# Kernel optimization log

Measured on AMD Instinct MI355X. Metric: run time of the kernel, lower is better.

## Reference

```python
import jax, jax.numpy as jnp
import numpy as np

EPS_SIM = 1e-10
EPS_NORM = 1e-12


def setup_inputs() -> dict:
    key = jax.random.key(0)
    k1, k2, k3, k4, k5 = jax.random.split(key, 5)
    B, CH, H, W = 64, 512, 28, 28
    R = CH // 16  # reduction
    x = jax.random.normal(k1, (B, CH, H, W), dtype=jnp.float32)
    # torch nn.Linear weights are [out, in]
    wD = jax.random.normal(k2, (R, CH), dtype=jnp.float32) * (1.0 / np.sqrt(CH))
    bD = jax.random.normal(k3, (R,), dtype=jnp.float32) * 0.01
    wU = jax.random.normal(k4, (CH, R), dtype=jnp.float32) * (1.0 / np.sqrt(R))
    bU = jax.random.normal(k5, (CH,), dtype=jnp.float32) * 0.01
    return {"x": x, "wD": wD, "bD": bD, "wU": wU, "bU": bU}


def _hybrid_weight(xap):
    # xap: [B, CH, N]; returns row-diag-masked, globally normalized similarity Wij [B, CH, CH]
    gram = jnp.einsum('bin,bjn->bij', xap, xap)           # [B,CH,CH]
    sq = jnp.sum(xap * xap, axis=-1)                      # [B,CH]
    d2 = sq[:, :, None] + sq[:, None, :] - 2.0 * gram
    d = jnp.sqrt(d2)
    d = jnp.where(jnp.isnan(d), 0.0, d)                   # NaN mask (sqrt of negatives)
    d = jnp.maximum(d, 0.0)                               # clamp(0, inf)
    mean_d = jnp.mean(d, axis=(1, 2), keepdims=True)
    l2_sim = jnp.exp(-d / (mean_d + EPS_SIM))
    w = jnp.sqrt(sq)                                      # per-channel L2 norm
    denom = jnp.maximum(w[:, :, None] * w[:, None, :], EPS_SIM)
    cos = gram / denom
    cos = jnp.where(jnp.isnan(cos), 0.0, cos)
    cos = jnp.maximum(cos, 0.0)
    sim = cos * l2_sim
    CH = sim.shape[1]
    sim = sim * (1.0 - jnp.eye(CH, dtype=sim.dtype))      # zero diagonal
    Wij = sim / (jnp.sum(sim, axis=(1, 2), keepdims=True) + EPS_SIM)
    return Wij


def reference(x, wD, bD, wU, bU):
    B, CH, H, W = x.shape
    r = 7  # rdim[512]
    # adaptive avg pool to 7x7 (H, W divisible by 7 -> exact block average)
    xap = x.reshape(B, CH, r, H // r, r, W // r).mean(axis=(3, 5)).reshape(B, CH, r * r)
    Wij = jax.lax.stop_gradient(_hybrid_weight(xap))      # computed under no_grad in torch
    gap = x.mean(axis=(2, 3))                             # [B,CH] global avg pool
    mu = gap.mean(axis=1, keepdims=True)
    std = jnp.std(gap, axis=1, ddof=1, keepdims=True)     # torch std is unbiased
    z = (gap - mu) / std                                  # [B,CH]
    # diag(z z^T Wij)_i = z_i * (z^T Wij)_i  -> avoid materializing zz^T
    local_mi = z * jnp.einsum('bj,bji->bi', z, Wij)       # [B,CH]
    m = local_mi.mean(axis=1, keepdims=True)
    s = jnp.std(local_mi, axis=1, ddof=1, keepdims=True)
    ch = (local_mi - m) / (s + EPS_NORM)                  # normal_G
    h = jax.nn.relu(ch @ wD.T + bD)
    att = h @ wU.T + bU
    scale = jax.nn.sigmoid(att)[:, :, None, None]
    return x * scale
```

## Files before the change

kernel.cpp:

```cpp
#include <hip/hip_runtime.h>
#include <hip/hip_bf16.h>
#include <stdint.h>

#define NB 64
#define NC 512
#define NHW 784
#define NK 49
#define KP 64
#define NR 32
#define NTASK 10

typedef short sh8 __attribute__((ext_vector_type(8)));
typedef float f32x4 __attribute__((ext_vector_type(4)));
typedef int v4i __attribute__((ext_vector_type(4)));

__device__ __forceinline__ float wave_sum(float v) {
#pragma unroll
  for (int o = 32; o; o >>= 1) v += __shfl_xor(v, o);
  return v;
}

__device__ __forceinline__ void task_decode(int s, int& ti, int& tj) {
  if (s < 4) { ti = 0; tj = s; }
  else if (s < 7) { ti = 1; tj = s - 3; }
  else if (s < 9) { ti = 2; tj = s - 5; }
  else { ti = 3; tj = 3; }
}

__global__ __launch_bounds__(256) void pool_kernel(const float* __restrict__ x,
                                                   __hip_bfloat16* __restrict__ xap,
                                                   float* __restrict__ wbuf,
                                                   float* __restrict__ gap) {
  __shared__ float sf[4][196];
  int t = threadIdx.x, wid = t >> 6, lane = t & 63;
  int row = blockIdx.x * 4 + wid;
  const f32x4* xr = (const f32x4*)(x + (size_t)row * NHW);
  f32x4 v0 = xr[lane];
  f32x4 v1 = xr[lane + 64];
  f32x4 v2 = xr[lane + 128];
  sf[wid][lane] = (v0.x + v0.y) + (v0.z + v0.w);
  sf[wid][lane + 64] = (v1.x + v1.y) + (v1.z + v1.w);
  sf[wid][lane + 128] = (v2.x + v2.y) + (v2.z + v2.w);
  if (lane < 4) {
    f32x4 v3 = xr[lane + 192];
    sf[wid][lane + 192] = (v3.x + v3.y) + (v3.z + v3.w);
  }
  __syncthreads();
  float bin = 0.f;
  if (lane < NK) {
    int pr = lane / 7, pc = lane - pr * 7;
    int f0 = pr * 28 + pc;
    bin = ((sf[wid][f0] + sf[wid][f0 + 7]) + (sf[wid][f0 + 14] + sf[wid][f0 + 21])) * 0.0625f;
  }
  float s1 = wave_sum(bin);
  float s2 = wave_sum(bin * bin);
  xap[(size_t)row * KP + lane] = __float2bfloat16(bin);
  if (lane == 0) {
    wbuf[row] = sqrtf(s2);
    gap[row] = s1 * (1.f / 49.f);
  }
}

__global__ __launch_bounds__(256) void meand_kernel(const __hip_bfloat16* __restrict__ xap,
                                                    const float* __restrict__ wbuf,
                                                    const float* __restrict__ gap,
                                                    float* __restrict__ dpart,
                                                    float* __restrict__ zbuf) {
  __shared__ __align__(16) __hip_bfloat16 Ab[128 * KP];
  __shared__ __align__(16) __hip_bfloat16 Bb[128 * KP];
  __shared__ float wiL[128], wjL[128];
  __shared__ float red[4];
  int blk = blockIdx.x;
  int b = blk / NTASK, s = blk - b * NTASK;
  int ti, tj;
  task_decode(s, ti, tj);
  bool diag = (ti == tj);
  int i0 = ti * 128, j0 = tj * 128;
  int t = threadIdx.x;
  int lane = t & 63, wave = t >> 6;
  const v4i* ga = (const v4i*)(xap + ((size_t)b * NC + i0) * KP);
  const v4i* gb = (const v4i*)(xap + ((size_t)b * NC + j0) * KP);
  v4i* la = (v4i*)Ab;
  v4i* lb = (v4i*)Bb;
#pragma unroll
  for (int q = 0; q < 4; ++q) {
    int cid = q * 256 + t;
    int r = cid >> 3, c = cid & 7;
    int dst = (r << 3) | (c ^ (r & 7));
    la[dst] = ga[cid];
    lb[dst] = gb[cid];
  }
  if (t < 128) {
    wiL[t] = wbuf[b * NC + i0 + t];
    wjL[t] = wbuf[b * NC + j0 + t];
  }
  if (s == 0) {
    float g0 = gap[b * NC + t], g1 = gap[b * NC + t + 256];
    float s1 = wave_sum(g0 + g1);
    if (lane == 0) red[wave] = s1;
    __syncthreads();
    float mu = ((red[0] + red[1]) + (red[2] + red[3])) * (1.f / 512.f);
    float e0 = g0 - mu, e1 = g1 - mu;
    __syncthreads();
    float vv = wave_sum(e0 * e0 + e1 * e1);
    if (lane == 0) red[wave] = vv;
    __syncthreads();
    float inv_sd = __builtin_amdgcn_rsqf(((red[0] + red[1]) + (red[2] + red[3])) * (1.f / 511.f));
    zbuf[b * NC + t] = e0 * inv_sd;
    zbuf[b * NC + t + 256] = e1 * inv_sd;
  }
  __syncthreads();
  int wi = wave >> 1, wn = wave & 1;
  int l15 = lane & 15, g16 = lane >> 4;
  sh8 af[4][2], bfr[4][2];
#pragma unroll
  for (int f = 0; f < 4; ++f) {
#pragma unroll
    for (int ks = 0; ks < 2; ++ks) {
      int ra = wi * 64 + f * 16 + l15;
      int rb = wn * 64 + f * 16 + l15;
      int cg2 = ks * 4 + g16;
      af[f][ks] = __builtin_bit_cast(sh8, ((const v4i*)Ab)[(ra << 3) | (cg2 ^ (ra & 7))]);
      bfr[f][ks] = __builtin_bit_cast(sh8, ((const v4i*)Bb)[(rb << 3) | (cg2 ^ (rb & 7))]);
    }
  }
  f32x4 acc[4][4];
#pragma unroll
  for (int fm = 0; fm < 4; ++fm)
#pragma unroll
    for (int fn = 0; fn < 4; ++fn) acc[fm][fn] = (f32x4){0.f, 0.f, 0.f, 0.f};
#pragma unroll
  for (int ks = 0; ks < 2; ++ks)
#pragma unroll
    for (int fm = 0; fm < 4; ++fm)
#pragma unroll
      for (int fn = 0; fn < 4; ++fn)
        acc[fm][fn] =
            __builtin_amdgcn_mfma_f32_16x16x32_bf16(af[fm][ks], bfr[fn][ks], acc[fm][fn], 0, 0, 0);
  float a2[4][4], b2[4];
#pragma unroll
  for (int fm = 0; fm < 4; ++fm)
#pragma unroll
    for (int rg = 0; rg < 4; ++rg) {
      float a = wiL[wi * 64 + fm * 16 + g16 * 4 + rg];
      a2[fm][rg] = a * a;
    }
#pragma unroll
  for (int fn = 0; fn < 4; ++fn) {
    float w = wjL[wn * 64 + fn * 16 + l15];
    b2[fn] = w * w;
  }
  float dsum = 0.f;
#pragma unroll
  for (int fm = 0; fm < 4; ++fm)
#pragma unroll
    for (int fn = 0; fn < 4; ++fn)
#pragma unroll
      for (int rg = 0; rg < 4; ++rg) {
        float d2 = fmaf(-2.f, acc[fm][fn][rg], a2[fm][rg] + b2[fn]);
        dsum += __builtin_amdgcn_sqrtf(fmaxf(d2, 0.f));
      }
  dsum = wave_sum(dsum);
  __syncthreads();
  if (lane == 0) red[wave] = dsum;
  __syncthreads();
  if (t == 0) dpart[blk] = ((red[0] + red[1]) + (red[2] + red[3])) * (diag ? 1.f : 2.f);
}

__global__ __launch_bounds__(256) void sim_kernel(const __hip_bfloat16* __restrict__ xap,
                                                  const float* __restrict__ wbuf,
                                                  const float* __restrict__ zbuf,
                                                  const float* __restrict__ dpart,
                                                  float* __restrict__ tpart,
                                                  float* __restrict__ spart) {
  __shared__ __align__(16) __hip_bfloat16 Ab[128 * KP];
  __shared__ __align__(16) __hip_bfloat16 Bb[128 * KP];
  __shared__ float wiL[128], wjL[128], zL[NC], tfull[NC];
  __shared__ float red[4];
  int blk = blockIdx.x;
  int b = blk / NTASK, s = blk - b * NTASK;
  int ti, tj;
  task_decode(s, ti, tj);
  bool diag = (ti == tj);
  int i0 = ti * 128, j0 = tj * 128;
  int t = threadIdx.x;
  int lane = t & 63, wave = t >> 6;
  float dsb = 0.f;
#pragma unroll
  for (int k = 0; k < NTASK; ++k) dsb += dpart[b * NTASK + k];
  float nim = -1.44269504f / (dsb * (1.f / 262144.f) + 1e-10f);
  const v4i* ga = (const v4i*)(xap + ((size_t)b * NC + i0) * KP);
  const v4i* gb = (const v4i*)(xap + ((size_t)b * NC + j0) * KP);
  v4i* la = (v4i*)Ab;
  v4i* lb = (v4i*)Bb;
#pragma unroll
  for (int q = 0; q < 4; ++q) {
    int cid = q * 256 + t;
    int r = cid >> 3, c = cid & 7;
    int dst = (r << 3) | (c ^ (r & 7));
    la[dst] = ga[cid];
    lb[dst] = gb[cid];
  }
  if (t < 128) {
    wiL[t] = wbuf[b * NC + i0 + t];
    wjL[t] = wbuf[b * NC + j0 + t];
  }
  zL[t] = zbuf[b * NC + t];
  zL[t + 256] = zbuf[b * NC + t + 256];
  tfull[t] = 0.f;
  tfull[t + 256] = 0.f;
  __syncthreads();
  int wi = wave >> 1, wn = wave & 1;
  int l15 = lane & 15, g16 = lane >> 4;
  sh8 af[4][2], bfr[4][2];
#pragma unroll
  for (int f = 0; f < 4; ++f) {
#pragma unroll
    for (int ks = 0; ks < 2; ++ks) {
      int ra = wi * 64 + f * 16 + l15;
      int rb = wn * 64 + f * 16 + l15;
      int cg2 = ks * 4 + g16;
      af[f][ks] = __builtin_bit_cast(sh8, ((const v4i*)Ab)[(ra << 3) | (cg2 ^ (ra & 7))]);
      bfr[f][ks] = __builtin_bit_cast(sh8, ((const v4i*)Bb)[(rb << 3) | (cg2 ^ (rb & 7))]);
    }
  }
  f32x4 acc[4][4];
#pragma unroll
  for (int fm = 0; fm < 4; ++fm)
#pragma unroll
    for (int fn = 0; fn < 4; ++fn) acc[fm][fn] = (f32x4){0.f, 0.f, 0.f, 0.f};
#pragma unroll
  for (int ks = 0; ks < 2; ++ks)
#pragma unroll
    for (int fm = 0; fm < 4; ++fm)
#pragma unroll
      for (int fn = 0; fn < 4; ++fn)
        acc[fm][fn] =
            __builtin_amdgcn_mfma_f32_16x16x32_bf16(af[fm][ks], bfr[fn][ks], acc[fm][fn], 0, 0, 0);
  float a2[4][4], ia[4][4], zi[4][4];
#pragma unroll
  for (int fm = 0; fm < 4; ++fm)
#pragma unroll
    for (int rg = 0; rg < 4; ++rg) {
      int il = wi * 64 + fm * 16 + g16 * 4 + rg;
      float a = wiL[il];
      a2[fm][rg] = a * a;
      ia[fm][rg] = __builtin_amdgcn_rcpf(fmaxf(a, 1e-7f));
      zi[fm][rg] = zL[i0 + il];
    }
  float b2[4], ib[4], zj[4];
#pragma unroll
  for (int fn = 0; fn < 4; ++fn) {
    int jl = wn * 64 + fn * 16 + l15;
    float w = wjL[jl];
    b2[fn] = w * w;
    ib[fn] = __builtin_amdgcn_rcpf(fmaxf(w, 1e-7f));
    zj[fn] = zL[j0 + jl];
  }
  float ssum = 0.f;
  float trow[4][4];
  float tcol[4] = {0.f, 0.f, 0.f, 0.f};
#pragma unroll
  for (int fm = 0; fm < 4; ++fm)
#pragma unroll
    for (int rg = 0; rg < 4; ++rg) trow[fm][rg] = 0.f;
#pragma unroll
  for (int fm = 0; fm < 4; ++fm)
#pragma unroll
    for (int fn = 0; fn < 4; ++fn) {
      float ibn = ib[fn];
#pragma unroll
      for (int rg = 0; rg < 4; ++rg) {
        float g = acc[fm][fn][rg];
        float d2 = fmaf(-2.f, g, a2[fm][rg] + b2[fn]);
        float d = __builtin_amdgcn_sqrtf(fmaxf(d2, 0.f));
        float sim = fmaxf(g, 0.f) * ia[fm][rg] * ibn * exp2f(d * nim);
        if (diag) {
          int il = wi * 64 + fm * 16 + g16 * 4 + rg;
          int jl = wn * 64 + fn * 16 + l15;
          if (il == jl) sim = 0.f;
        }
        ssum += sim;
        trow[fm][rg] = fmaf(sim, zj[fn], trow[fm][rg]);
        tcol[fn] = fmaf(sim, zi[fm][rg], tcol[fn]);
      }
    }
#pragma unroll
  for (int fm = 0; fm < 4; ++fm)
#pragma unroll
    for (int rg = 0; rg < 4; ++rg) {
      float v = trow[fm][rg];
#pragma unroll
      for (int o = 8; o; o >>= 1) v += __shfl_xor(v, o);
      if (l15 == 0) atomicAdd(&tfull[i0 + wi * 64 + fm * 16 + g16 * 4 + rg], v);
    }
  if (!diag) {
#pragma unroll
    for (int fn = 0; fn < 4; ++fn) {
      float v = tcol[fn];
      v += __shfl_xor(v, 16);
      v += __shfl_xor(v, 32);
      if (g16 == 0) atomicAdd(&tfull[j0 + wn * 64 + fn * 16 + l15], v);
    }
  }
  ssum = wave_sum(ssum);
  if (lane == 0) red[wave] = ssum;
  __syncthreads();
  if (t == 0) spart[blk] = ((red[0] + red[1]) + (red[2] + red[3])) * (diag ? 1.f : 2.f);
  tpart[(size_t)blk * NC + t] = tfull[t];
  tpart[(size_t)blk * NC + t + 256] = tfull[t + 256];
}

__global__ __launch_bounds__(256) void mlp_kernel(const float* __restrict__ zbuf,
                                                  const float* __restrict__ tpart,
                                                  const float* __restrict__ spart,
                                                  const float* __restrict__ wD,
                                                  const float* __restrict__ bD,
                                                  const float* __restrict__ wU,
                                                  const float* __restrict__ bU,
                                                  float* __restrict__ scl) {
  __shared__ float red[4];
  __shared__ float chL[NC];
  __shared__ float hL[NR];
  int b = blockIdx.x, t = threadIdx.x;
  int lane = t & 63, wid = t >> 6;
  float S = 0.f;
#pragma unroll
  for (int k = 0; k < NTASK; ++k) S += spart[b * NTASK + k];
  float invS = 1.f / (S + 1e-10f);
  float t0 = 0.f, t1 = 0.f;
#pragma unroll
  for (int j = 0; j < NTASK; ++j) {
    t0 += tpart[((size_t)b * NTASK + j) * NC + t];
    t1 += tpart[((size_t)b * NTASK + j) * NC + t + 256];
  }
  float lm0 = zbuf[b * NC + t] * t0 * invS;
  float lm1 = zbuf[b * NC + t + 256] * t1 * invS;
  float s2 = wave_sum(lm0 + lm1);
  if (lane == 0) red[wid] = s2;
  __syncthreads();
  float m = ((red[0] + red[1]) + (red[2] + red[3])) * (1.f / 512.f);
  float d0 = lm0 - m, d1 = lm1 - m;
  __syncthreads();
  float v2 = wave_sum(d0 * d0 + d1 * d1);
  if (lane == 0) red[wid] = v2;
  __syncthreads();
  float isd2 = __builtin_amdgcn_rcpf(
      sqrtf(((red[0] + red[1]) + (red[2] + red[3])) * (1.f / 511.f)) + 1e-12f);
  chL[t] = d0 * isd2;
  chL[t + 256] = d1 * isd2;
  __syncthreads();
  int k = t >> 3, p = t & 7;
  const float* wrow = wD + k * NC + p * 64;
  const float* cp = chL + p * 64;
  float hp = 0.f;
#pragma unroll
  for (int i = 0; i < 64; ++i) hp += wrow[i] * cp[i];
#pragma unroll
  for (int o = 4; o; o >>= 1) hp += __shfl_xor(hp, o);
  if (p == 0) hL[k] = fmaxf(hp + bD[k], 0.f);
  __syncthreads();
#pragma unroll
  for (int u = 0; u < 2; ++u) {
    int c = t + u * 256;
    const float* wrU = wU + c * NR;
    float att = bU[c];
#pragma unroll
    for (int kk = 0; kk < NR; ++kk) att += hL[kk] * wrU[kk];
    scl[b * NC + c] = __builtin_amdgcn_rcpf(1.f + __expf(-att));
  }
}

__global__ __launch_bounds__(256) void scale_kernel(const float* __restrict__ x,
                                                    const float* __restrict__ scl,
                                                    float* __restrict__ out) {
  unsigned idx = blockIdx.x * 256u + threadIdx.x;
  unsigned row = idx / 196u;
  float s = scl[row];
  f32x4 v = ((const f32x4*)x)[idx];
  v *= s;
  __builtin_nontemporal_store(v, ((f32x4*)out) + idx);
}

extern "C" void kernel_launch(void* const* d_in, const int* in_sizes, int n_in,
                              void* d_out, int out_size, void* d_ws, size_t ws_size,
                              hipStream_t stream) {
  const float* x = (const float*)d_in[0];
  const float* wD = (const float*)d_in[1];
  const float* bD = (const float*)d_in[2];
  const float* wU = (const float*)d_in[3];
  const float* bU = (const float*)d_in[4];
  float* out = (float*)d_out;
  char* ws = (char*)d_ws;

  __hip_bfloat16* xap = (__hip_bfloat16*)ws;
  float* fbase = (float*)(ws + (size_t)NB * NC * KP * 2);
  float* wbuf = fbase;
  float* gap = wbuf + NB * NC;
  float* dpart = gap + NB * NC;
  float* spart = dpart + NB * NTASK;
  float* tpart = spart + NB * NTASK;
  float* scl = tpart + NB * NTASK * NC;
  float* zbuf = scl + NB * NC;

  hipLaunchKernelGGL(pool_kernel, dim3(NB * NC / 4), dim3(256), 0, stream, x, xap, wbuf, gap);
  hipLaunchKernelGGL(meand_kernel, dim3(NB * NTASK), dim3(256), 0, stream, xap, wbuf, gap, dpart,
                     zbuf);
  hipLaunchKernelGGL(sim_kernel, dim3(NB * NTASK), dim3(256), 0, stream, xap, wbuf, zbuf, dpart,
                     tpart, spart);
  hipLaunchKernelGGL(mlp_kernel, dim3(NB), dim3(256), 0, stream, zbuf, tpart, spart, wD, bD, wU,
                     bU, scl);
  hipLaunchKernelGGL(scale_kernel, dim3(25088), dim3(256), 0, stream, x, scl, out);
}
```

Before: 82.31 us.

## Fuse distance, similarity and MLP stages into one per-batch kernel

Replaces the meand, sim and mlp kernels with a single 1024-thread block per batch that keeps the pooled bf16 features, z-scores and accumulators in shared memory. The block loops over all ten upper-triangle tiles twice, first for the mean distance and then for the similarity, with block-level reductions in between. This removes two kernel launches and the global partial-sum round-trips. In exchange, only 64 blocks run the middle stage, which lowers parallelism and serialises the tile work inside each block.

```diff
diff --git a/kernel.cpp b/kernel.cpp
--- a/kernel.cpp
+++ b/kernel.cpp
@@ -61,313 +61,263 @@
   }
 }
 
-__global__ __launch_bounds__(256) void meand_kernel(const __hip_bfloat16* __restrict__ xap,
-                                                    const float* __restrict__ wbuf,
-                                                    const float* __restrict__ gap,
-                                                    float* __restrict__ dpart,
-                                                    float* __restrict__ zbuf) {
-  __shared__ __align__(16) __hip_bfloat16 Ab[128 * KP];
-  __shared__ __align__(16) __hip_bfloat16 Bb[128 * KP];
-  __shared__ float wiL[128], wjL[128];
-  __shared__ float red[4];
-  int blk = blockIdx.x;
-  int b = blk / NTASK, s = blk - b * NTASK;
-  int ti, tj;
-  task_decode(s, ti, tj);
-  bool diag = (ti == tj);
-  int i0 = ti * 128, j0 = tj * 128;
-  int t = threadIdx.x;
-  int lane = t & 63, wave = t >> 6;
-  const v4i* ga = (const v4i*)(xap + ((size_t)b * NC + i0) * KP);
-  const v4i* gb = (const v4i*)(xap + ((size_t)b * NC + j0) * KP);
-  v4i* la = (v4i*)Ab;
-  v4i* lb = (v4i*)Bb;
-#pragma unroll
-  for (int q = 0; q < 4; ++q) {
-    int cid = q * 256 + t;
-    int r = cid >> 3, c = cid & 7;
-    int dst = (r << 3) | (c ^ (r & 7));
-    la[dst] = ga[cid];
-    lb[dst] = gb[cid];
-  }
-  if (t < 128) {
-    wiL[t] = wbuf[b * NC + i0 + t];
-    wjL[t] = wbuf[b * NC + j0 + t];
-  }
-  if (s == 0) {
-    float g0 = gap[b * NC + t], g1 = gap[b * NC + t + 256];
-    float s1 = wave_sum(g0 + g1);
-    if (lane == 0) red[wave] = s1;
-    __syncthreads();
-    float mu = ((red[0] + red[1]) + (red[2] + red[3])) * (1.f / 512.f);
-    float e0 = g0 - mu, e1 = g1 - mu;
-    __syncthreads();
-    float vv = wave_sum(e0 * e0 + e1 * e1);
-    if (lane == 0) red[wave] = vv;
-    __syncthreads();
-    float inv_sd = __builtin_amdgcn_rsqf(((red[0] + red[1]) + (red[2] + red[3])) * (1.f / 511.f));
-    zbuf[b * NC + t] = e0 * inv_sd;
-    zbuf[b * NC + t + 256] = e1 * inv_sd;
-  }
-  __syncthreads();
-  int wi = wave >> 1, wn = wave & 1;
-  int l15 = lane & 15, g16 = lane >> 4;
-  sh8 af[4][2], bfr[4][2];
-#pragma unroll
-  for (int f = 0; f < 4; ++f) {
-#pragma unroll
-    for (int ks = 0; ks < 2; ++ks) {
-      int ra = wi * 64 + f * 16 + l15;
-      int rb = wn * 64 + f * 16 + l15;
-      int cg2 = ks * 4 + g16;
-      af[f][ks] = __builtin_bit_cast(sh8, ((const v4i*)Ab)[(ra << 3) | (cg2 ^ (ra & 7))]);
-      bfr[f][ks] = __builtin_bit_cast(sh8, ((const v4i*)Bb)[(rb << 3) | (cg2 ^ (rb & 7))]);
-    }
-  }
-  f32x4 acc[4][4];
-#pragma unroll
-  for (int fm = 0; fm < 4; ++fm)
-#pragma unroll
-    for (int fn = 0; fn < 4; ++fn) acc[fm][fn] = (f32x4){0.f, 0.f, 0.f, 0.f};
-#pragma unroll
-  for (int ks = 0; ks < 2; ++ks)
-#pragma unroll
-    for (int fm = 0; fm < 4; ++fm)
-#pragma unroll
-      for (int fn = 0; fn < 4; ++fn)
-        acc[fm][fn] =
-            __builtin_amdgcn_mfma_f32_16x16x32_bf16(af[fm][ks], bfr[fn][ks], acc[fm][fn], 0, 0, 0);
-  float a2[4][4], b2[4];
-#pragma unroll
-  for (int fm = 0; fm < 4; ++fm)
-#pragma unroll
-    for (int rg = 0; rg < 4; ++rg) {
-      float a = wiL[wi * 64 + fm * 16 + g16 * 4 + rg];
-      a2[fm][rg] = a * a;
-    }
-#pragma unroll
-  for (int fn = 0; fn < 4; ++fn) {
-    float w = wjL[wn * 64 + fn * 16 + l15];
-    b2[fn] = w * w;
-  }
-  float dsum = 0.f;
-#pragma unroll
-  for (int fm = 0; fm < 4; ++fm)
-#pragma unroll
-    for (int fn = 0; fn < 4; ++fn)
-#pragma unroll
-      for (int rg = 0; rg < 4; ++rg) {
-        float d2 = fmaf(-2.f, acc[fm][fn][rg], a2[fm][rg] + b2[fn]);
-        dsum += __builtin_amdgcn_sqrtf(fmaxf(d2, 0.f));
-      }
-  dsum = wave_sum(dsum);
-  __syncthreads();
-  if (lane == 0) red[wave] = dsum;
-  __syncthreads();
-  if (t == 0) dpart[blk] = ((red[0] + red[1]) + (red[2] + red[3])) * (diag ? 1.f : 2.f);
-}
-
-__global__ __launch_bounds__(256) void sim_kernel(const __hip_bfloat16* __restrict__ xap,
-                                                  const float* __restrict__ wbuf,
-                                                  const float* __restrict__ zbuf,
-                                                  const float* __restrict__ dpart,
-                                                  float* __restrict__ tpart,
-                                                  float* __restrict__ spart) {
-  __shared__ __align__(16) __hip_bfloat16 Ab[128 * KP];
-  __shared__ __align__(16) __hip_bfloat16 Bb[128 * KP];
-  __shared__ float wiL[128], wjL[128], zL[NC], tfull[NC];
-  __shared__ float red[4];
-  int blk = blockIdx.x;
-  int b = blk / NTASK, s = blk - b * NTASK;
-  int ti, tj;
-  task_decode(s, ti, tj);
-  bool diag = (ti == tj);
-  int i0 = ti * 128, j0 = tj * 128;
-  int t = threadIdx.x;
-  int lane = t & 63, wave = t >> 6;
-  float dsb = 0.f;
-#pragma unroll
-  for (int k = 0; k < NTASK; ++k) dsb += dpart[b * NTASK + k];
-  float nim = -1.44269504f / (dsb * (1.f / 262144.f) + 1e-10f);
-  const v4i* ga = (const v4i*)(xap + ((size_t)b * NC + i0) * KP);
-  const v4i* gb = (const v4i*)(xap + ((size_t)b * NC + j0) * KP);
-  v4i* la = (v4i*)Ab;
-  v4i* lb = (v4i*)Bb;
-#pragma unroll
-  for (int q = 0; q < 4; ++q) {
-    int cid = q * 256 + t;
-    int r = cid >> 3, c = cid & 7;
-    int dst = (r << 3) | (c ^ (r & 7));
-    la[dst] = ga[cid];
-    lb[dst] = gb[cid];
-  }
-  if (t < 128) {
-    wiL[t] = wbuf[b * NC + i0 + t];
-    wjL[t] = wbuf[b * NC + j0 + t];
-  }
-  zL[t] = zbuf[b * NC + t];
-  zL[t + 256] = zbuf[b * NC + t + 256];
-  tfull[t] = 0.f;
-  tfull[t + 256] = 0.f;
-  __syncthreads();
-  int wi = wave >> 1, wn = wave & 1;
-  int l15 = lane & 15, g16 = lane >> 4;
-  sh8 af[4][2], bfr[4][2];
-#pragma unroll
-  for (int f = 0; f < 4; ++f) {
-#pragma unroll
-    for (int ks = 0; ks < 2; ++ks) {
-      int ra = wi * 64 + f * 16 + l15;
-      int rb = wn * 64 + f * 16 + l15;
-      int cg2 = ks * 4 + g16;
-      af[f][ks] = __builtin_bit_cast(sh8, ((const v4i*)Ab)[(ra << 3) | (cg2 ^ (ra & 7))]);
-      bfr[f][ks] = __builtin_bit_cast(sh8, ((const v4i*)Bb)[(rb << 3) | (cg2 ^ (rb & 7))]);
-    }
-  }
-  f32x4 acc[4][4];
-#pragma unroll
-  for (int fm = 0; fm < 4; ++fm)
-#pragma unroll
-    for (int fn = 0; fn < 4; ++fn) acc[fm][fn] = (f32x4){0.f, 0.f, 0.f, 0.f};
-#pragma unroll
-  for (int ks = 0; ks < 2; ++ks)
-#pragma unroll
-    for (int fm = 0; fm < 4; ++fm)
-#pragma unroll
-      for (int fn = 0; fn < 4; ++fn)
-        acc[fm][fn] =
-            __builtin_amdgcn_mfma_f32_16x16x32_bf16(af[fm][ks], bfr[fn][ks], acc[fm][fn], 0, 0, 0);
-  float a2[4][4], ia[4][4], zi[4][4];
-#pragma unroll
-  for (int fm = 0; fm < 4; ++fm)
-#pragma unroll
-    for (int rg = 0; rg < 4; ++rg) {
-      int il = wi * 64 + fm * 16 + g16 * 4 + rg;
-      float a = wiL[il];
-      a2[fm][rg] = a * a;
-      ia[fm][rg] = __builtin_amdgcn_rcpf(fmaxf(a, 1e-7f));
-      zi[fm][rg] = zL[i0 + il];
-    }
-  float b2[4], ib[4], zj[4];
-#pragma unroll
-  for (int fn = 0; fn < 4; ++fn) {
-    int jl = wn * 64 + fn * 16 + l15;
-    float w = wjL[jl];
-    b2[fn] = w * w;
-    ib[fn] = __builtin_amdgcn_rcpf(fmaxf(w, 1e-7f));
-    zj[fn] = zL[j0 + jl];
-  }
-  float ssum = 0.f;
-  float trow[4][4];
-  float tcol[4] = {0.f, 0.f, 0.f, 0.f};
-#pragma unroll
-  for (int fm = 0; fm < 4; ++fm)
-#pragma unroll
-    for (int rg = 0; rg < 4; ++rg) trow[fm][rg] = 0.f;
-#pragma unroll
-  for (int fm = 0; fm < 4; ++fm)
-#pragma unroll
-    for (int fn = 0; fn < 4; ++fn) {
-      float ibn = ib[fn];
-#pragma unroll
-      for (int rg = 0; rg < 4; ++rg) {
-        float g = acc[fm][fn][rg];
-        float d2 = fmaf(-2.f, g, a2[fm][rg] + b2[fn]);
-        float d = __builtin_amdgcn_sqrtf(fmaxf(d2, 0.f));
-        float sim = fmaxf(g, 0.f) * ia[fm][rg] * ibn * exp2f(d * nim);
-        if (diag) {
-          int il = wi * 64 + fm * 16 + g16 * 4 + rg;
-          int jl = wn * 64 + fn * 16 + l15;
-          if (il == jl) sim = 0.f;
-        }
-        ssum += sim;
-        trow[fm][rg] = fmaf(sim, zj[fn], trow[fm][rg]);
-        tcol[fn] = fmaf(sim, zi[fm][rg], tcol[fn]);
-      }
-    }
-#pragma unroll
-  for (int fm = 0; fm < 4; ++fm)
-#pragma unroll
-    for (int rg = 0; rg < 4; ++rg) {
-      float v = trow[fm][rg];
-#pragma unroll
-      for (int o = 8; o; o >>= 1) v += __shfl_xor(v, o);
-      if (l15 == 0) atomicAdd(&tfull[i0 + wi * 64 + fm * 16 + g16 * 4 + rg], v);
-    }
-  if (!diag) {
-#pragma unroll
-    for (int fn = 0; fn < 4; ++fn) {
-      float v = tcol[fn];
-      v += __shfl_xor(v, 16);
-      v += __shfl_xor(v, 32);
-      if (g16 == 0) atomicAdd(&tfull[j0 + wn * 64 + fn * 16 + l15], v);
-    }
-  }
-  ssum = wave_sum(ssum);
-  if (lane == 0) red[wave] = ssum;
-  __syncthreads();
-  if (t == 0) spart[blk] = ((red[0] + red[1]) + (red[2] + red[3])) * (diag ? 1.f : 2.f);
-  tpart[(size_t)blk * NC + t] = tfull[t];
-  tpart[(size_t)blk * NC + t + 256] = tfull[t + 256];
-}
-
-__global__ __launch_bounds__(256) void mlp_kernel(const float* __restrict__ zbuf,
-                                                  const float* __restrict__ tpart,
-                                                  const float* __restrict__ spart,
-                                                  const float* __restrict__ wD,
-                                                  const float* __restrict__ bD,
-                                                  const float* __restrict__ wU,
-                                                  const float* __restrict__ bU,
-                                                  float* __restrict__ scl) {
-  __shared__ float red[4];
-  __shared__ float chL[NC];
+__global__ __launch_bounds__(1024) void middle_kernel(
+    const __hip_bfloat16* __restrict__ xap, const float* __restrict__ wbuf,
+    const float* __restrict__ gap, const float* __restrict__ wD,
+    const float* __restrict__ bD, const float* __restrict__ wU,
+    const float* __restrict__ bU, float* __restrict__ scl) {
+  __shared__ __align__(16) __hip_bfloat16 X[NC * KP];
+  __shared__ float wL[NC], zL[NC], tfull[NC], chL[NC];
+  __shared__ float red[16];
   __shared__ float hL[NR];
   int b = blockIdx.x, t = threadIdx.x;
-  int lane = t & 63, wid = t >> 6;
+  int lane = t & 63, w = t >> 6;
+  const v4i* gx = (const v4i*)(xap + (size_t)b * NC * KP);
+  v4i* lx = (v4i*)X;
+#pragma unroll
+  for (int q = 0; q < 4; ++q) {
+    int cid = q * 1024 + t;
+    int r = cid >> 3, c = cid & 7;
+    lx[(r << 3) | (c ^ (r & 7))] = gx[cid];
+  }
+  if (t < NC) {
+    wL[t] = wbuf[b * NC + t];
+    tfull[t] = 0.f;
+  }
+  float g0 = (t < NC) ? gap[b * NC + t] : 0.f;
+  float s1 = wave_sum(g0);
+  if (lane == 0) red[w] = s1;
+  __syncthreads();
+  float mu = 0.f;
+#pragma unroll
+  for (int i = 0; i < 16; ++i) mu += red[i];
+  mu *= (1.f / 512.f);
+  float e0 = g0 - mu;
+  float dd = (t < NC) ? e0 * e0 : 0.f;
+  __syncthreads();
+  float vv = wave_sum(dd);
+  if (lane == 0) red[w] = vv;
+  __syncthreads();
+  float var = 0.f;
+#pragma unroll
+  for (int i = 0; i < 16; ++i) var += red[i];
+  float inv_sd = __builtin_amdgcn_rsqf(var * (1.f / 511.f));
+  if (t < NC) zL[t] = e0 * inv_sd;
+  __syncthreads();
+
+  int wi = w >> 2, wn = w & 3;
+  int l15 = lane & 15, g16 = lane >> 4;
+  const v4i* lxc = (const v4i*)X;
+
+  float dacc = 0.f;
+#pragma unroll 1
+  for (int s = 0; s < NTASK; ++s) {
+    int ti, tj;
+    task_decode(s, ti, tj);
+    int i0 = ti * 128, j0 = tj * 128;
+    sh8 af[2][2], bfr[2][2];
+#pragma unroll
+    for (int f = 0; f < 2; ++f)
+#pragma unroll
+      for (int ks = 0; ks < 2; ++ks) {
+        int ra = i0 + wi * 32 + f * 16 + l15;
+        int rb = j0 + wn * 32 + f * 16 + l15;
+        int cg = ks * 4 + g16;
+        af[f][ks] = __builtin_bit_cast(sh8, lxc[(ra << 3) | (cg ^ (ra & 7))]);
+        bfr[f][ks] = __builtin_bit_cast(sh8, lxc[(rb << 3) | (cg ^ (rb & 7))]);
+      }
+    f32x4 acc[2][2];
+#pragma unroll
+    for (int fm = 0; fm < 2; ++fm)
+#pragma unroll
+      for (int fn = 0; fn < 2; ++fn) acc[fm][fn] = (f32x4){0.f, 0.f, 0.f, 0.f};
+#pragma unroll
+    for (int ks = 0; ks < 2; ++ks)
+#pragma unroll
+      for (int fm = 0; fm < 2; ++fm)
+#pragma unroll
+        for (int fn = 0; fn < 2; ++fn)
+          acc[fm][fn] = __builtin_amdgcn_mfma_f32_16x16x32_bf16(af[fm][ks], bfr[fn][ks],
+                                                                acc[fm][fn], 0, 0, 0);
+    float a2[2][4], b2v[2];
+#pragma unroll
+    for (int fm = 0; fm < 2; ++fm)
+#pragma unroll
+      for (int rg = 0; rg < 4; ++rg) {
+        float a = wL[i0 + wi * 32 + fm * 16 + g16 * 4 + rg];
+        a2[fm][rg] = a * a;
+      }
+#pragma unroll
+    for (int fn = 0; fn < 2; ++fn) {
+      float ww = wL[j0 + wn * 32 + fn * 16 + l15];
+      b2v[fn] = ww * ww;
+    }
+    float dsum = 0.f;
+#pragma unroll
+    for (int fm = 0; fm < 2; ++fm)
+#pragma unroll
+      for (int fn = 0; fn < 2; ++fn)
+#pragma unroll
+        for (int rg = 0; rg < 4; ++rg) {
+          float d2 = fmaf(-2.f, acc[fm][fn][rg], a2[fm][rg] + b2v[fn]);
+          dsum += __builtin_amdgcn_sqrtf(fmaxf(d2, 0.f));
+        }
+    dacc += dsum * ((ti == tj) ? 1.f : 2.f);
+  }
+  dacc = wave_sum(dacc);
+  __syncthreads();
+  if (lane == 0) red[w] = dacc;
+  __syncthreads();
+  float sD = 0.f;
+#pragma unroll
+  for (int i = 0; i < 16; ++i) sD += red[i];
+  float nim = -1.44269504f / (sD * (1.f / 262144.f) + 1e-10f);
+
+  float ssacc = 0.f;
+#pragma unroll 1
+  for (int s = 0; s < NTASK; ++s) {
+    int ti, tj;
+    task_decode(s, ti, tj);
+    bool diag = (ti == tj);
+    int i0 = ti * 128, j0 = tj * 128;
+    sh8 af[2][2], bfr[2][2];
+#pragma unroll
+    for (int f = 0; f < 2; ++f)
+#pragma unroll
+      for (int ks = 0; ks < 2; ++ks) {
+        int ra = i0 + wi * 32 + f * 16 + l15;
+        int rb = j0 + wn * 32 + f * 16 + l15;
+        int cg = ks * 4 + g16;
+        af[f][ks] = __builtin_bit_cast(sh8, lxc[(ra << 3) | (cg ^ (ra & 7))]);
+        bfr[f][ks] = __builtin_bit_cast(sh8, lxc[(rb << 3) | (cg ^ (rb & 7))]);
+      }
+    f32x4 acc[2][2];
+#pragma unroll
+    for (int fm = 0; fm < 2; ++fm)
+#pragma unroll
+      for (int fn = 0; fn < 2; ++fn) acc[fm][fn] = (f32x4){0.f, 0.f, 0.f, 0.f};
+#pragma unroll
+    for (int ks = 0; ks < 2; ++ks)
+#pragma unroll
+      for (int fm = 0; fm < 2; ++fm)
+#pragma unroll
+        for (int fn = 0; fn < 2; ++fn)
+          acc[fm][fn] = __builtin_amdgcn_mfma_f32_16x16x32_bf16(af[fm][ks], bfr[fn][ks],
+                                                                acc[fm][fn], 0, 0, 0);
+    float a2[2][4], ia[2][4], zi[2][4];
+#pragma unroll
+    for (int fm = 0; fm < 2; ++fm)
+#pragma unroll
+      for (int rg = 0; rg < 4; ++rg) {
+        int il = wi * 32 + fm * 16 + g16 * 4 + rg;
+        float a = wL[i0 + il];
+        a2[fm][rg] = a * a;
+        ia[fm][rg] = __builtin_amdgcn_rcpf(fmaxf(a, 1e-7f));
+        zi[fm][rg] = zL[i0 + il];
+      }
+    float b2v[2], ib[2], zj[2];
+#pragma unroll
+    for (int fn = 0; fn < 2; ++fn) {
+      int jl = wn * 32 + fn * 16 + l15;
+      float ww = wL[j0 + jl];
+      b2v[fn] = ww * ww;
+      ib[fn] = __builtin_amdgcn_rcpf(fmaxf(ww, 1e-7f));
+      zj[fn] = zL[j0 + jl];
+    }
+    float ssum = 0.f;
+    float trow[2][4];
+    float tcol[2] = {0.f, 0.f};
+#pragma unroll
+    for (int fm = 0; fm < 2; ++fm)
+#pragma unroll
+      for (int rg = 0; rg < 4; ++rg) trow[fm][rg] = 0.f;
+#pragma unroll
+    for (int fm = 0; fm < 2; ++fm)
+#pragma unroll
+      for (int fn = 0; fn < 2; ++fn) {
+        float ibn = ib[fn];
+#pragma unroll
+        for (int rg = 0; rg < 4; ++rg) {
+          float g = acc[fm][fn][rg];
+          float d2 = fmaf(-2.f, g, a2[fm][rg] + b2v[fn]);
+          float d = __builtin_amdgcn_sqrtf(fmaxf(d2, 0.f));
+          float sim = fmaxf(g, 0.f) * ia[fm][rg] * ibn * exp2f(d * nim);
+          if (diag) {
+            int il = wi * 32 + fm * 16 + g16 * 4 + rg;
+            int jl = wn * 32 + fn * 16 + l15;
+            if (il == jl) sim = 0.f;
+          }
+          ssum += sim;
+          trow[fm][rg] = fmaf(sim, zj[fn], trow[fm][rg]);
+          tcol[fn] = fmaf(sim, zi[fm][rg], tcol[fn]);
+        }
+      }
+#pragma unroll
+    for (int fm = 0; fm < 2; ++fm)
+#pragma unroll
+      for (int rg = 0; rg < 4; ++rg) {
+        float v = trow[fm][rg];
+#pragma unroll
+        for (int o = 8; o; o >>= 1) v += __shfl_xor(v, o);
+        if (l15 == 0) atomicAdd(&tfull[i0 + wi * 32 + fm * 16 + g16 * 4 + rg], v);
+      }
+    if (!diag) {
+#pragma unroll
+      for (int fn = 0; fn < 2; ++fn) {
+        float v = tcol[fn];
+        v += __shfl_xor(v, 16);
+        v += __shfl_xor(v, 32);
+        if (g16 == 0) atomicAdd(&tfull[j0 + wn * 32 + fn * 16 + l15], v);
+      }
+    }
+    ssacc += ssum * (diag ? 1.f : 2.f);
+  }
+  ssacc = wave_sum(ssacc);
+  __syncthreads();
+  if (lane == 0) red[w] = ssacc;
+  __syncthreads();
   float S = 0.f;
 #pragma unroll
-  for (int k = 0; k < NTASK; ++k) S += spart[b * NTASK + k];
+  for (int i = 0; i < 16; ++i) S += red[i];
   float invS = 1.f / (S + 1e-10f);
-  float t0 = 0.f, t1 = 0.f;
-#pragma unroll
-  for (int j = 0; j < NTASK; ++j) {
-    t0 += tpart[((size_t)b * NTASK + j) * NC + t];
-    t1 += tpart[((size_t)b * NTASK + j) * NC + t + 256];
-  }
-  float lm0 = zbuf[b * NC + t] * t0 * invS;
-  float lm1 = zbuf[b * NC + t + 256] * t1 * invS;
-  float s2 = wave_sum(lm0 + lm1);
-  if (lane == 0) red[wid] = s2;
-  __syncthreads();
-  float m = ((red[0] + red[1]) + (red[2] + red[3])) * (1.f / 512.f);
-  float d0 = lm0 - m, d1 = lm1 - m;
-  __syncthreads();
-  float v2 = wave_sum(d0 * d0 + d1 * d1);
-  if (lane == 0) red[wid] = v2;
-  __syncthreads();
-  float isd2 = __builtin_amdgcn_rcpf(
-      sqrtf(((red[0] + red[1]) + (red[2] + red[3])) * (1.f / 511.f)) + 1e-12f);
-  chL[t] = d0 * isd2;
-  chL[t + 256] = d1 * isd2;
-  __syncthreads();
-  int k = t >> 3, p = t & 7;
-  const float* wrow = wD + k * NC + p * 64;
-  const float* cp = chL + p * 64;
+
+  float lm = (t < NC) ? zL[t] * tfull[t] * invS : 0.f;
+  float q3 = wave_sum(lm);
+  __syncthreads();
+  if (lane == 0) red[w] = q3;
+  __syncthreads();
+  float m_ = 0.f;
+#pragma unroll
+  for (int i = 0; i < 16; ++i) m_ += red[i];
+  m_ *= (1.f / 512.f);
+  float d0 = lm - m_;
+  float dd2 = (t < NC) ? d0 * d0 : 0.f;
+  float vv2 = wave_sum(dd2);
+  __syncthreads();
+  if (lane == 0) red[w] = vv2;
+  __syncthreads();
+  float v2s = 0.f;
+#pragma unroll
+  for (int i = 0; i < 16; ++i) v2s += red[i];
+  float isd2 = __builtin_amdgcn_rcpf(sqrtf(v2s * (1.f / 511.f)) + 1e-12f);
+  if (t < NC) chL[t] = d0 * isd2;
+  __syncthreads();
+  int k = t >> 5, p = t & 31;
+  const float* wrow = wD + k * NC + p * 16;
+  const float* cp = chL + p * 16;
   float hp = 0.f;
 #pragma unroll
-  for (int i = 0; i < 64; ++i) hp += wrow[i] * cp[i];
-#pragma unroll
-  for (int o = 4; o; o >>= 1) hp += __shfl_xor(hp, o);
+  for (int i = 0; i < 16; ++i) hp += wrow[i] * cp[i];
+#pragma unroll
+  for (int o = 16; o; o >>= 1) hp += __shfl_xor(hp, o);
   if (p == 0) hL[k] = fmaxf(hp + bD[k], 0.f);
   __syncthreads();
-#pragma unroll
-  for (int u = 0; u < 2; ++u) {
-    int c = t + u * 256;
-    const float* wrU = wU + c * NR;
-    float att = bU[c];
+  if (t < NC) {
+    const float* wrU = wU + t * NR;
+    float att = bU[t];
 #pragma unroll
     for (int kk = 0; kk < NR; ++kk) att += hL[kk] * wrU[kk];
-    scl[b * NC + c] = __builtin_amdgcn_rcpf(1.f + __expf(-att));
+    scl[b * NC + t] = __builtin_amdgcn_rcpf(1.f + __expf(-att));
   }
 }
 
@@ -397,18 +347,10 @@
   float* fbase = (float*)(ws + (size_t)NB * NC * KP * 2);
   float* wbuf = fbase;
   float* gap = wbuf + NB * NC;
-  float* dpart = gap + NB * NC;
-  float* spart = dpart + NB * NTASK;
-  float* tpart = spart + NB * NTASK;
-  float* scl = tpart + NB * NTASK * NC;
-  float* zbuf = scl + NB * NC;
+  float* scl = gap + NB * NC;
 
   hipLaunchKernelGGL(pool_kernel, dim3(NB * NC / 4), dim3(256), 0, stream, x, xap, wbuf, gap);
-  hipLaunchKernelGGL(meand_kernel, dim3(NB * NTASK), dim3(256), 0, stream, xap, wbuf, gap, dpart,
-                     zbuf);
-  hipLaunchKernelGGL(sim_kernel, dim3(NB * NTASK), dim3(256), 0, stream, xap, wbuf, zbuf, dpart,
-                     tpart, spart);
-  hipLaunchKernelGGL(mlp_kernel, dim3(NB), dim3(256), 0, stream, zbuf, tpart, spart, wD, bD, wU,
+  hipLaunchKernelGGL(middle_kernel, dim3(NB), dim3(1024), 0, stream, xap, wbuf, gap, wD, bD, wU,
                      bU, scl);
   hipLaunchKernelGGL(scale_kernel, dim3(25088), dim3(256), 0, stream, x, scl, out);
 }
```

Measured after the change: 103.9 us. 26.3% more time.
